# Kernel optimization log

Hardware: AMD Instinct MI355X
Metric: run time of the kernel (lower is better)

## Reference

```python
import jax, jax.numpy as jnp
import numpy as np

K = 2  # number of SGConv propagation hops


def setup_inputs() -> dict:
    key = jax.random.key(0)
    k1, k2, k3, k4 = jax.random.split(key, 4)
    N, E, T, H = 50000, 800000, 256, 128
    x = jax.random.normal(k1, (N, T), dtype=jnp.float32)
    edge_index = jax.random.randint(k2, (2, E), 0, N, dtype=jnp.int64)
    edge_weights = jax.random.normal(k3, (E,), dtype=jnp.float32)
    W = jax.random.normal(k4, (H, T), dtype=jnp.float32) * 0.05
    b = jnp.zeros((H,), dtype=jnp.float32)
    return {"x": x, "edge_index": edge_index, "edge_weights": edge_weights, "W": W, "b": b}


def reference(x, edge_index, edge_weights, W, b):
    N = x.shape[0]
    # in-place clamp from forward(): weights with elu(w) <= 0 are set to 1e-7
    ew = jnp.where(jax.nn.elu(edge_weights) <= 0, jnp.float32(1e-7), edge_weights)

    # gcn_norm with add_self_loops=True (fill_value = 1.0)
    loop = jnp.arange(N, dtype=edge_index.dtype)
    row = jnp.concatenate([edge_index[0], loop])  # source nodes
    col = jnp.concatenate([edge_index[1], loop])  # target nodes (aggregation index)
    w = jnp.concatenate([ew, jnp.ones((N,), dtype=ew.dtype)])

    deg = jax.ops.segment_sum(w, col, num_segments=N)          # [N]
    dis = jnp.where(deg > 0, jax.lax.rsqrt(deg), jnp.float32(0.0))
    norm = dis[row] * w * dis[col]                             # [E+N]

    # K-hop propagation: h <- scatter_add(norm * h[src]) at dst
    h = x
    for _ in range(K):
        h = jax.ops.segment_sum(h[row] * norm[:, None], col, num_segments=N)

    # final linear transform of SGConv
    return h @ W.T + b
```

## Files before the change

kernel.cpp:

```cpp
#include <hip/hip_runtime.h>


typedef __attribute__((ext_vector_type(8))) short short8_t;
typedef __attribute__((ext_vector_type(4))) float f32x4_t;

constexpr int BK    = 256;
constexpr int CAP   = 8192;
constexpr int CHUNK = 4096;

__device__ inline unsigned short f2bf(float f) {
    unsigned int u = __float_as_uint(f);
    return (unsigned short)((u + 0x7fffu + ((u >> 16) & 1u)) >> 16);
}
__device__ inline float bf_lo(unsigned int u) { return __uint_as_float(u << 16); }
__device__ inline float bf_hi(unsigned int u) { return __uint_as_float(u & 0xffff0000u); }

__device__ inline void async_load16(const void* g, void* l) {
    __builtin_amdgcn_global_load_lds(
        (const __attribute__((address_space(1))) unsigned int*)g,
        (__attribute__((address_space(3))) unsigned int*)l, 16, 0, 0);
}

__global__ __launch_bounds__(256) void k_zero(int* __restrict__ p, int n)
{
    int i = blockIdx.x * 256 + threadIdx.x;
    if (i < n) p[i] = 0;
}

__global__ __launch_bounds__(256) void k_passA(
    const int* __restrict__ rows, const int* __restrict__ cols,
    const float* __restrict__ ew, int E,
    unsigned int* __restrict__ bwr,
    unsigned char* __restrict__ bcl,
    int* __restrict__ tails,
    const float* __restrict__ W, unsigned short* __restrict__ Wbf, int WT)
{
    const int tid = threadIdx.x;
    const int gid = blockIdx.x * 256 + tid;
    if (gid < WT) Wbf[gid] = f2bf(W[gid]);

    __shared__ unsigned short lcol[CHUNK], lrow[CHUNK], lw[CHUNK];
    __shared__ unsigned short sidx[CHUNK];
    __shared__ int hist[256], lofs[256], fill[256], gbase[256];

    const int e0  = blockIdx.x * CHUNK;
    const int cnt = min(CHUNK, E - e0);
    if (cnt <= 0) return;

    hist[tid] = 0; fill[tid] = 0;
    __syncthreads();

    for (int i = tid; i < cnt; i += 256) {
        const int c = cols[e0 + i];
        const int r = rows[e0 + i];
        float w = ew[e0 + i];
        w = (w > 0.0f) ? w : 1e-7f;
        lcol[i] = (unsigned short)c;
        lrow[i] = (unsigned short)r;
        lw[i]   = f2bf(w);
        atomicAdd(&hist[c >> 8], 1);
    }
    __syncthreads();

    {
        const int v = hist[tid];
        lofs[tid] = v;
        __syncthreads();
        for (int off = 1; off < 256; off <<= 1) {
            int t = (tid >= off) ? lofs[tid - off] : 0;
            __syncthreads();
            lofs[tid] += t;
            __syncthreads();
        }
        const int excl = lofs[tid] - v;
        __syncthreads();
        lofs[tid] = excl;
        __syncthreads();
    }

    for (int i = tid; i < cnt; i += 256) {
        const int b = lcol[i] >> 8;
        const int pos = lofs[b] + atomicAdd(&fill[b], 1);
        sidx[pos] = (unsigned short)i;
    }
    __syncthreads();

    {
        const int h = hist[tid];
        gbase[tid] = (h > 0) ? atomicAdd(&tails[tid], h) : 0;
    }
    __syncthreads();

    for (int i = tid; i < cnt; i += 256) {
        const int e = sidx[i];
        const int b = lcol[e] >> 8;
        const int slot = gbase[b] + (i - lofs[b]);
        if (slot < CAP) {
            const int addr = b * CAP + slot;
            bwr[addr] = ((unsigned int)lw[e] << 16) | lrow[e];
            bcl[addr] = (unsigned char)(lcol[e] & 255);
        }
    }
}

__global__ __launch_bounds__(256) void k_passB(
    const unsigned int* __restrict__ bwr, const unsigned char* __restrict__ bcl,
    const int* __restrict__ tails,
    unsigned int* __restrict__ meta, int* __restrict__ starts,
    int* __restrict__ ends, float* __restrict__ dis, int N)
{
    const int tid  = threadIdx.x;
    const int b    = blockIdx.x;
    const int base = b * CAP;
    const int cnt  = min(tails[b], CAP);

    __shared__ unsigned int  lwr[CAP];
    __shared__ unsigned char lcl[CAP];
    __shared__ unsigned int  srt[CAP];
    __shared__ int hist[256], offs[256], fill[256];

    hist[tid] = 0; fill[tid] = 0;
    __syncthreads();

    for (int i = tid; i < cnt; i += 256) {
        lwr[i] = bwr[base + i];
        unsigned char c = bcl[base + i];
        lcl[i] = c;
        atomicAdd(&hist[c], 1);
    }
    __syncthreads();

    {
        const int v = hist[tid];
        offs[tid] = v;
        __syncthreads();
        for (int off = 1; off < 256; off <<= 1) {
            int t = (tid >= off) ? offs[tid - off] : 0;
            __syncthreads();
            offs[tid] += t;
            __syncthreads();
        }
        const int excl = offs[tid] - v;
        __syncthreads();
        offs[tid] = excl;
        __syncthreads();
    }

    for (int i = tid; i < cnt; i += 256) {
        const int c = lcl[i];
        const int pos = offs[c] + atomicAdd(&fill[c], 1);
        srt[pos] = lwr[i];
    }
    __syncthreads();

    for (int i = tid; i < cnt; i += 256) meta[base + i] = srt[i];

    const int node = b * BK + tid;
    if (node < N) {
        const int s = offs[tid];
        const int t = s + hist[tid];
        float sum = 1.0f;
        for (int j = s; j < t; ++j) sum += bf_hi(srt[j]);
        dis[node]    = rsqrtf(sum);
        starts[node] = base + s;
        ends[node]   = base + t;
    }
}

__global__ __launch_bounds__(256, 2) void k_transform_mfma(
    const float* __restrict__ x, const unsigned short* __restrict__ Wbf,
    const float* __restrict__ dis, unsigned short* __restrict__ z, int N)
{
    constexpr int RB = 32;
    __shared__ float xs[RB][256];

    const int tid  = threadIdx.x;
    const int r0   = blockIdx.x * RB;
    const int wave = tid >> 6;
    const int lane = tid & 63;
    const int lr   = lane & 15;
    const int kg   = lane >> 4;
    const int nb   = (wave & 1) * 4;
    const int wr0  = (wave >> 1) * 16;

#pragma unroll
    for (int r = 0; r < 8; ++r) {
        const int row  = wave * 8 + r;
        const int grow = r0 + row;
        if (grow < N) {
            const char* src = (const char*)(x + (size_t)grow * 256)
                              + ((lane * 16) ^ ((row & 7) << 4));
            async_load16(src, &xs[row][0]);
        } else {
            *(float4*)((char*)&xs[row][0] + lane * 16) =
                make_float4(0.f, 0.f, 0.f, 0.f);
        }
    }

    short8_t wf[4][8];
#pragma unroll
    for (int n = 0; n < 4; ++n)
#pragma unroll
        for (int k = 0; k < 8; ++k)
            wf[n][k] = *reinterpret_cast<const short8_t*>(
                Wbf + (size_t)((nb + n) * 16 + lr) * 256 + k * 32 + kg * 8);

    __syncthreads();

    f32x4_t acc[4];
#pragma unroll
    for (int n = 0; n < 4; ++n) acc[n] = (f32x4_t){0.f, 0.f, 0.f, 0.f};

    const char* xb = (const char*)&xs[0][0];
    const int   row = wr0 + lr;
    const int   sw  = (row & 7) << 4;

#pragma unroll
    for (int k = 0; k < 8; ++k) {
        const int g  = k * 128 + kg * 32;
        const int a0 = row * 1024 + (g ^ sw);
        const int a1 = row * 1024 + ((g + 16) ^ sw);
        float4 f0 = *(const float4*)(xb + a0);
        float4 f1 = *(const float4*)(xb + a1);
        short8_t af;
        af[0] = (short)f2bf(f0.x); af[1] = (short)f2bf(f0.y);
        af[2] = (short)f2bf(f0.z); af[3] = (short)f2bf(f0.w);
        af[4] = (short)f2bf(f1.x); af[5] = (short)f2bf(f1.y);
        af[6] = (short)f2bf(f1.z); af[7] = (short)f2bf(f1.w);
#pragma unroll
        for (int n = 0; n < 4; ++n)
            acc[n] = __builtin_amdgcn_mfma_f32_16x16x32_bf16(af, wf[n][k],
                                                             acc[n], 0, 0, 0);
    }

    float dsc[4];
#pragma unroll
    for (int r = 0; r < 4; ++r) {
        const int orow = r0 + wr0 + kg * 4 + r;
        dsc[r] = (orow < N) ? dis[orow] : 0.f;
    }
#pragma unroll
    for (int n = 0; n < 4; ++n) {
#pragma unroll
        for (int r = 0; r < 4; ++r) {
            const int orow = r0 + wr0 + kg * 4 + r;
            if (orow < N)
                z[(size_t)orow * 128 + (nb + n) * 16 + lr] =
                    f2bf(dsc[r] * acc[n][r]);
        }
    }
}

template <bool FINAL>
__global__ __launch_bounds__(256) void k_hop(
    const int* __restrict__ starts, const int* __restrict__ ends,
    const unsigned int* __restrict__ meta,
    const float* __restrict__ dis, const unsigned int* __restrict__ hin,
    const float* __restrict__ bias, void* __restrict__ hout, int N)
{
    const int wave = threadIdx.x >> 6;
    const int lane = threadIdx.x & 63;
    const int node = blockIdx.x * 4 + wave;
    if (node >= N) return;

    const int s = __builtin_amdgcn_readfirstlane(starts[node]);
    const int t = __builtin_amdgcn_readfirstlane(ends[node]);
    const float d = dis[node];

    unsigned int v = hin[(size_t)node * 64 + lane];
    float ax = bf_lo(v), ay = bf_hi(v);

    int j = s;
    for (; j + 8 <= t; j += 8) {
        unsigned int m0 = meta[j],     m1 = meta[j + 1];
        unsigned int m2 = meta[j + 2], m3 = meta[j + 3];
        unsigned int m4 = meta[j + 4], m5 = meta[j + 5];
        unsigned int m6 = meta[j + 6], m7 = meta[j + 7];
        unsigned int u0 = hin[(size_t)(m0 & 0xffffu) * 64 + lane];
        unsigned int u1 = hin[(size_t)(m1 & 0xffffu) * 64 + lane];
        unsigned int u2 = hin[(size_t)(m2 & 0xffffu) * 64 + lane];
        unsigned int u3 = hin[(size_t)(m3 & 0xffffu) * 64 + lane];
        unsigned int u4 = hin[(size_t)(m4 & 0xffffu) * 64 + lane];
        unsigned int u5 = hin[(size_t)(m5 & 0xffffu) * 64 + lane];
        unsigned int u6 = hin[(size_t)(m6 & 0xffffu) * 64 + lane];
        unsigned int u7 = hin[(size_t)(m7 & 0xffffu) * 64 + lane];
        ax += bf_hi(m0) * bf_lo(u0); ay += bf_hi(m0) * bf_hi(u0);
        ax += bf_hi(m1) * bf_lo(u1); ay += bf_hi(m1) * bf_hi(u1);
        ax += bf_hi(m2) * bf_lo(u2); ay += bf_hi(m2) * bf_hi(u2);
        ax += bf_hi(m3) * bf_lo(u3); ay += bf_hi(m3) * bf_hi(u3);
        ax += bf_hi(m4) * bf_lo(u4); ay += bf_hi(m4) * bf_hi(u4);
        ax += bf_hi(m5) * bf_lo(u5); ay += bf_hi(m5) * bf_hi(u5);
        ax += bf_hi(m6) * bf_lo(u6); ay += bf_hi(m6) * bf_hi(u6);
        ax += bf_hi(m7) * bf_lo(u7); ay += bf_hi(m7) * bf_hi(u7);
    }
    for (; j < t; ++j) {
        unsigned int m = meta[j];
        const float w = bf_hi(m);
        unsigned int u = hin[(size_t)(m & 0xffffu) * 64 + lane];
        ax += w * bf_lo(u); ay += w * bf_hi(u);
    }

    if (FINAL) {
        float2 bv = reinterpret_cast<const float2*>(bias)[lane];
        float2 o; o.x = d * ax + bv.x; o.y = d * ay + bv.y;
        reinterpret_cast<float2*>(hout)[(size_t)node * 64 + lane] = o;
    } else {
        const float d2 = d * d;
        unsigned int p = (unsigned int)f2bf(d2 * ax) |
                         ((unsigned int)f2bf(d2 * ay) << 16);
        reinterpret_cast<unsigned int*>(hout)[(size_t)node * 64 + lane] = p;
    }
}

extern "C" void kernel_launch(void* const* d_in, const int* in_sizes, int n_in,
                              void* d_out, int out_size, void* d_ws, size_t ws_size,
                              hipStream_t stream)
{
    const float* x  = (const float*)d_in[0];
    const int*   ei = (const int*)d_in[1];
    const float* ew = (const float*)d_in[2];
    const float* W  = (const float*)d_in[3];
    const float* b  = (const float*)d_in[4];

    const int E  = in_sizes[2];
    const int H  = in_sizes[4];
    const int T  = in_sizes[3] / H;
    const int N  = in_sizes[0] / T;
    const int WT = in_sizes[3];
    const int NB = (N + BK - 1) / BK;

    const int* rows = ei;
    const int* cols = ei + E;

    char* wsb = (char*)d_ws;
    unsigned int*   z    = (unsigned int*)wsb;   wsb += (size_t)N * (H / 2) * 4;
    unsigned int*   z1   = (unsigned int*)wsb;   wsb += (size_t)N * (H / 2) * 4;
    unsigned int*   meta = (unsigned int*)wsb;   wsb += (size_t)NB * CAP * 4;
    unsigned short* Wbf  = (unsigned short*)wsb; wsb += (size_t)WT * 2;
    float*          dis  = (float*)wsb;          wsb += (size_t)N * 4;
    int*            sta  = (int*)wsb;            wsb += (size_t)N * 4;
    int*            end_ = (int*)wsb;            wsb += (size_t)N * 4;
    int*            tails= (int*)wsb;            wsb += (size_t)NB * 4;
    unsigned int*   bwr  = z1;
    unsigned char*  bcl  = (unsigned char*)(z1 + (size_t)NB * CAP);

    float* out = (float*)d_out;

    k_zero<<<(NB + 255) / 256, 256, 0, stream>>>(tails, NB);
    {
        const int nblkA = (E + CHUNK - 1) / CHUNK;
        k_passA<<<nblkA, 256, 0, stream>>>(rows, cols, ew, E,
                                           bwr, bcl, tails, W, Wbf, WT);
        k_passB<<<NB, 256, 0, stream>>>(bwr, bcl, tails,
                                        meta, sta, end_, dis, N);
    }

    {
        const int RB = 32;
        k_transform_mfma<<<(N + RB - 1) / RB, 256, 0, stream>>>(
            x, Wbf, dis, (unsigned short*)z, N);
    }

    const int gH = (N + 3) / 4;
    k_hop<false><<<gH, 256, 0, stream>>>(sta, end_, meta, dis, z, nullptr, z1, N);
    k_hop<true ><<<gH, 256, 0, stream>>>(sta, end_, meta, dis, z1, b, out, N);
}
```

Before: 139.4 us.

## Permute hidden columns in z to pack 8-byte stores, unpermute in final hop

The transform kernel now writes each row's four MFMA output columns as one packed 8-byte store instead of four scattered 2-byte stores. This stores z in a permuted column order, and the final hop maps each lane back to the true column indices when writing the output and reading the bias. It also drops the register preload of W fragments in favour of loading them inside the k loop, and removes the occupancy hint from the launch bounds to cut register pressure. The risk is more global or L2 traffic for W and uncoalesced scalar output stores in the final hop.

```diff
diff --git a/kernel.cpp b/kernel.cpp
--- a/kernel.cpp
+++ b/kernel.cpp
@@ -167,9 +167,9 @@
     }
 }
 
-__global__ __launch_bounds__(256, 2) void k_transform_mfma(
+__global__ __launch_bounds__(256) void k_transform_mfma(
     const float* __restrict__ x, const unsigned short* __restrict__ Wbf,
-    const float* __restrict__ dis, unsigned short* __restrict__ z, int N)
+    const float* __restrict__ dis, void* __restrict__ z, int N)
 {
     constexpr int RB = 32;
     __shared__ float xs[RB][256];
@@ -196,22 +196,13 @@
                 make_float4(0.f, 0.f, 0.f, 0.f);
         }
     }
-
-    short8_t wf[4][8];
-#pragma unroll
-    for (int n = 0; n < 4; ++n)
-#pragma unroll
-        for (int k = 0; k < 8; ++k)
-            wf[n][k] = *reinterpret_cast<const short8_t*>(
-                Wbf + (size_t)((nb + n) * 16 + lr) * 256 + k * 32 + kg * 8);
-
     __syncthreads();
 
     f32x4_t acc[4];
 #pragma unroll
     for (int n = 0; n < 4; ++n) acc[n] = (f32x4_t){0.f, 0.f, 0.f, 0.f};
 
-    const char* xb = (const char*)&xs[0][0];
+    const char* xb  = (const char*)&xs[0][0];
     const int   row = wr0 + lr;
     const int   sw  = (row & 7) << 4;
 
@@ -228,11 +219,15 @@
         af[4] = (short)f2bf(f1.x); af[5] = (short)f2bf(f1.y);
         af[6] = (short)f2bf(f1.z); af[7] = (short)f2bf(f1.w);
 #pragma unroll
-        for (int n = 0; n < 4; ++n)
-            acc[n] = __builtin_amdgcn_mfma_f32_16x16x32_bf16(af, wf[n][k],
+        for (int n = 0; n < 4; ++n) {
+            const short8_t bf = *reinterpret_cast<const short8_t*>(
+                Wbf + (size_t)((nb + n) * 16 + lr) * 256 + k * 32 + kg * 8);
+            acc[n] = __builtin_amdgcn_mfma_f32_16x16x32_bf16(af, bf,
                                                              acc[n], 0, 0, 0);
-    }
-
+        }
+    }
+
+    char* zb = (char*)z;
     float dsc[4];
 #pragma unroll
     for (int r = 0; r < 4; ++r) {
@@ -240,13 +235,16 @@
         dsc[r] = (orow < N) ? dis[orow] : 0.f;
     }
 #pragma unroll
-    for (int n = 0; n < 4; ++n) {
-#pragma unroll
-        for (int r = 0; r < 4; ++r) {
-            const int orow = r0 + wr0 + kg * 4 + r;
-            if (orow < N)
-                z[(size_t)orow * 128 + (nb + n) * 16 + lr] =
-                    f2bf(dsc[r] * acc[n][r]);
+    for (int r = 0; r < 4; ++r) {
+        const int orow = r0 + wr0 + kg * 4 + r;
+        if (orow < N) {
+            const float s = dsc[r];
+            unsigned int lo = (unsigned int)f2bf(s * acc[0][r]) |
+                              ((unsigned int)f2bf(s * acc[1][r]) << 16);
+            unsigned int hi = (unsigned int)f2bf(s * acc[2][r]) |
+                              ((unsigned int)f2bf(s * acc[3][r]) << 16);
+            *(uint2*)(zb + (size_t)orow * 256 + (wave & 1) * 128 + lr * 8) =
+                make_uint2(lo, hi);
         }
     }
 }
@@ -301,9 +299,11 @@
     }
 
     if (FINAL) {
-        float2 bv = reinterpret_cast<const float2*>(bias)[lane];
-        float2 o; o.x = d * ax + bv.x; o.y = d * ay + bv.y;
-        reinterpret_cast<float2*>(hout)[(size_t)node * 64 + lane] = o;
+        const int c0 = ((lane & 32) ? 64 : 0) + 32 * (lane & 1) +
+                       ((lane & 31) >> 1);
+        float* orow = (float*)hout + (size_t)node * 128;
+        orow[c0]      = d * ax + bias[c0];
+        orow[c0 + 16] = d * ay + bias[c0 + 16];
     } else {
         const float d2 = d * d;
         unsigned int p = (unsigned int)f2bf(d2 * ax) |
@@ -358,7 +358,7 @@
     {
         const int RB = 32;
         k_transform_mfma<<<(N + RB - 1) / RB, 256, 0, stream>>>(
-            x, Wbf, dis, (unsigned short*)z, N);
+            x, Wbf, dis, z, N);
     }
 
     const int gH = (N + 3) / 4;
```

Result: faster. 135.3 us (-2.9%).

## Transpose transform MFMA for packed stores and predicate hop tail into one batch

Applied to the files above, without the earlier changes.

The transform kernel now swaps MFMA operands so W rows form the A operand and x rows the B operand. Each lane ends up holding consecutive output features, so it writes packed uint2 bf16 pairs instead of scattered 16-bit stores. The output columns are split across a second grid dimension, which halves per-thread W fragment registers but loads the x tile twice. The hop kernel's scalar remainder loop becomes one predicated batch of up to eight gathers, so the tail loads can be issued in parallel.

```diff
diff --git a/kernel.cpp b/kernel.cpp
--- a/kernel.cpp
+++ b/kernel.cpp
@@ -167,21 +167,21 @@
     }
 }
 
-__global__ __launch_bounds__(256, 2) void k_transform_mfma(
+__global__ __launch_bounds__(256) void k_transform_mfma(
     const float* __restrict__ x, const unsigned short* __restrict__ Wbf,
-    const float* __restrict__ dis, unsigned short* __restrict__ z, int N)
+    const float* __restrict__ dis, unsigned int* __restrict__ z, int N)
 {
     constexpr int RB = 32;
     __shared__ float xs[RB][256];
 
     const int tid  = threadIdx.x;
     const int r0   = blockIdx.x * RB;
+    const int hb   = blockIdx.y;
     const int wave = tid >> 6;
     const int lane = tid & 63;
     const int lr   = lane & 15;
     const int kg   = lane >> 4;
-    const int nb   = (wave & 1) * 4;
-    const int wr0  = (wave >> 1) * 16;
+    const int wrow = hb * 64 + wave * 16 + lr;
 
 #pragma unroll
     for (int r = 0; r < 8; ++r) {
@@ -197,56 +197,44 @@
         }
     }
 
-    short8_t wf[4][8];
-#pragma unroll
-    for (int n = 0; n < 4; ++n)
-#pragma unroll
-        for (int k = 0; k < 8; ++k)
-            wf[n][k] = *reinterpret_cast<const short8_t*>(
-                Wbf + (size_t)((nb + n) * 16 + lr) * 256 + k * 32 + kg * 8);
-
-    __syncthreads();
-
-    f32x4_t acc[4];
-#pragma unroll
-    for (int n = 0; n < 4; ++n) acc[n] = (f32x4_t){0.f, 0.f, 0.f, 0.f};
+    short8_t wf[8];
+#pragma unroll
+    for (int k = 0; k < 8; ++k)
+        wf[k] = *reinterpret_cast<const short8_t*>(
+            Wbf + (size_t)wrow * 256 + k * 32 + kg * 8);
+
+    __syncthreads();
 
     const char* xb = (const char*)&xs[0][0];
-    const int   row = wr0 + lr;
-    const int   sw  = (row & 7) << 4;
-
-#pragma unroll
-    for (int k = 0; k < 8; ++k) {
-        const int g  = k * 128 + kg * 32;
-        const int a0 = row * 1024 + (g ^ sw);
-        const int a1 = row * 1024 + ((g + 16) ^ sw);
-        float4 f0 = *(const float4*)(xb + a0);
-        float4 f1 = *(const float4*)(xb + a1);
-        short8_t af;
-        af[0] = (short)f2bf(f0.x); af[1] = (short)f2bf(f0.y);
-        af[2] = (short)f2bf(f0.z); af[3] = (short)f2bf(f0.w);
-        af[4] = (short)f2bf(f1.x); af[5] = (short)f2bf(f1.y);
-        af[6] = (short)f2bf(f1.z); af[7] = (short)f2bf(f1.w);
-#pragma unroll
-        for (int n = 0; n < 4; ++n)
-            acc[n] = __builtin_amdgcn_mfma_f32_16x16x32_bf16(af, wf[n][k],
-                                                             acc[n], 0, 0, 0);
-    }
-
-    float dsc[4];
-#pragma unroll
-    for (int r = 0; r < 4; ++r) {
-        const int orow = r0 + wr0 + kg * 4 + r;
-        dsc[r] = (orow < N) ? dis[orow] : 0.f;
-    }
-#pragma unroll
-    for (int n = 0; n < 4; ++n) {
-#pragma unroll
-        for (int r = 0; r < 4; ++r) {
-            const int orow = r0 + wr0 + kg * 4 + r;
-            if (orow < N)
-                z[(size_t)orow * 128 + (nb + n) * 16 + lr] =
-                    f2bf(dsc[r] * acc[n][r]);
+
+#pragma unroll
+    for (int xt = 0; xt < 2; ++xt) {
+        f32x4_t acc = (f32x4_t){0.f, 0.f, 0.f, 0.f};
+        const int xrow = xt * 16 + lr;
+        const int sw   = (xrow & 7) << 4;
+#pragma unroll
+        for (int k = 0; k < 8; ++k) {
+            const int g  = k * 128 + kg * 32;
+            const int a0 = xrow * 1024 + (g ^ sw);
+            const int a1 = xrow * 1024 + ((g + 16) ^ sw);
+            float4 f0 = *(const float4*)(xb + a0);
+            float4 f1 = *(const float4*)(xb + a1);
+            short8_t bf;
+            bf[0] = (short)f2bf(f0.x); bf[1] = (short)f2bf(f0.y);
+            bf[2] = (short)f2bf(f0.z); bf[3] = (short)f2bf(f0.w);
+            bf[4] = (short)f2bf(f1.x); bf[5] = (short)f2bf(f1.y);
+            bf[6] = (short)f2bf(f1.z); bf[7] = (short)f2bf(f1.w);
+            acc = __builtin_amdgcn_mfma_f32_16x16x32_bf16(wf[k], bf, acc, 0, 0, 0);
+        }
+        const int node = r0 + xrow;
+        if (node < N) {
+            const float d = dis[node];
+            unsigned int lo = (unsigned int)f2bf(d * acc[0]) |
+                              ((unsigned int)f2bf(d * acc[1]) << 16);
+            unsigned int hi = (unsigned int)f2bf(d * acc[2]) |
+                              ((unsigned int)f2bf(d * acc[3]) << 16);
+            *(uint2*)(&z[(size_t)node * 64 + hb * 32 + wave * 8 + kg * 2]) =
+                make_uint2(lo, hi);
         }
     }
 }
@@ -293,11 +281,24 @@
         ax += bf_hi(m6) * bf_lo(u6); ay += bf_hi(m6) * bf_hi(u6);
         ax += bf_hi(m7) * bf_lo(u7); ay += bf_hi(m7) * bf_hi(u7);
     }
-    for (; j < t; ++j) {
-        unsigned int m = meta[j];
-        const float w = bf_hi(m);
-        unsigned int u = hin[(size_t)(m & 0xffffu) * 64 + lane];
-        ax += w * bf_lo(u); ay += w * bf_hi(u);
+    if (j < t) {
+        unsigned int mm[8];
+        float        ww[8];
+#pragma unroll
+        for (int u = 0; u < 8; ++u) {
+            const int jj = j + u;
+            mm[u] = meta[(jj < t) ? jj : (t - 1)];
+            ww[u] = (jj < t) ? bf_hi(mm[u]) : 0.0f;
+        }
+        unsigned int uu[8];
+#pragma unroll
+        for (int u = 0; u < 8; ++u)
+            uu[u] = hin[(size_t)(mm[u] & 0xffffu) * 64 + lane];
+#pragma unroll
+        for (int u = 0; u < 8; ++u) {
+            ax += ww[u] * bf_lo(uu[u]);
+            ay += ww[u] * bf_hi(uu[u]);
+        }
     }
 
     if (FINAL) {
@@ -357,8 +358,8 @@
 
     {
         const int RB = 32;
-        k_transform_mfma<<<(N + RB - 1) / RB, 256, 0, stream>>>(
-            x, Wbf, dis, (unsigned short*)z, N);
+        dim3 grid((N + RB - 1) / RB, 2);
+        k_transform_mfma<<<grid, 256, 0, stream>>>(x, Wbf, dis, z, N);
     }
 
     const int gH = (N + 3) / 4;
```

Result: faster. 121.7 us (-12.7%).
